# Kernel optimization log

Hardware: AMD Instinct MI355X
Metric: run time of the kernel (lower is better)

## Reference

```python
import jax, jax.numpy as jnp
import numpy as np

N = 4096  # query nodes
L = 4096  # source nodes
C = 512   # in_channels == out_channels (required by the original code path)
H = 8     # num_heads
DK = C // H  # 64


def setup_inputs() -> dict:
    key = jax.random.key(0)
    ks = jax.random.split(key, 12)
    s = 1.0 / np.sqrt(C)
    return {
        "query_input": jax.random.normal(ks[0], (N, C), jnp.float32),
        "source_input": jax.random.normal(ks[1], (L, C), jnp.float32),
        # outer value projection (TransConvLayerGAT.Wv): C -> C
        "Wv_out_w": jax.random.uniform(ks[2], (C, C), jnp.float32, -s, s),
        "Wv_out_b": jax.random.uniform(ks[3], (C,), jnp.float32, -s, s),
        # attention projections
        "Wq_w": jax.random.uniform(ks[4], (C, H * DK), jnp.float32, -s, s),
        "Wq_b": jax.random.uniform(ks[5], (H * DK,), jnp.float32, -s, s),
        "Wk_w": jax.random.uniform(ks[6], (C, H * DK), jnp.float32, -s, s),
        "Wk_b": jax.random.uniform(ks[7], (H * DK,), jnp.float32, -s, s),
        # attention value projection: C -> H * out_channels
        "Wv_attn_w": jax.random.uniform(ks[8], (C, H * C), jnp.float32, -s, s),
        "Wv_attn_b": jax.random.uniform(ks[9], (H * C,), jnp.float32, -s, s),
    }


def reference(query_input, source_input, Wv_out_w, Wv_out_b,
              Wq_w, Wq_b, Wk_w, Wk_b, Wv_attn_w, Wv_attn_b):
    # outer value projection (use_weight=True)
    value = source_input @ Wv_out_w + Wv_out_b            # [L, C]
    # attention projections
    q = (query_input @ Wq_w + Wq_b).reshape(N, H, DK)     # [N, H, DK]
    k = (source_input @ Wk_w + Wk_b).reshape(L, H, DK)    # [L, H, DK]
    v = (value @ Wv_attn_w + Wv_attn_b).reshape(L, H, C)  # [L, H, C]
    scale = 1.0 / jnp.sqrt(jnp.float32(DK))
    scores = jnp.einsum('nhm,lhm->nlh', q, k) * scale     # [N, L, H]
    # NOTE: faithful to original — softmax over the HEADS axis (dim=-1)
    w = jax.nn.softmax(scores, axis=-1)                   # [N, L, H]
    out = jnp.einsum('nlh,lhd->nhd', w, v)                # [N, H, C]
    return out
```

## Files before the change

### kernel.cpp

```cpp
#include <hip/hip_runtime.h>
#include <cstddef>
#include <cstdint>

#define NQ 4096
#define NS 4096
#define CH 512
#define NH 8
#define HC 4096

typedef unsigned short u16;
typedef __attribute__((ext_vector_type(8))) short short8;
typedef __attribute__((ext_vector_type(4))) float f32x4;

__device__ __forceinline__ u16 f2b(float f) {
  unsigned u = __float_as_uint(f);
  return (u16)((u + 0x7fffu + ((u >> 16) & 1u)) >> 16);
}
__device__ __forceinline__ f32x4 mfma16(short8 a, short8 b, f32x4 c) {
  return __builtin_amdgcn_mfma_f32_16x16x32_bf16(a, b, c, 0, 0, 0);
}
__device__ __forceinline__ void gload_lds16(const void* g, void* l) {
  __builtin_amdgcn_global_load_lds(
      (const __attribute__((address_space(1))) void*)g,
      (__attribute__((address_space(3))) void*)l, 16, 0, 0);
}

__global__ __launch_bounds__(256) void convert_flat(
    const float* __restrict__ in, u16* __restrict__ out, int n4)
{
  int idx = blockIdx.x * 256 + threadIdx.x;
  int stride = gridDim.x * 256;
  for (int i = idx; i < n4; i += stride) {
    float4 v = ((const float4*)in)[i];
    ushort4 o;
    o.x = f2b(v.x); o.y = f2b(v.y); o.z = f2b(v.z); o.w = f2b(v.w);
    ((ushort4*)out)[i] = o;
  }
}

__global__ __launch_bounds__(256) void transpose_convert(
    const float* __restrict__ in, u16* __restrict__ out, int R, int C)
{
  __shared__ u16 tile[32][33];
  int tid = threadIdx.x;
  int tx = tid & 31, ty = tid >> 5;
#pragma unroll
  for (int i = 0; i < 4; ++i) {
    int r = blockIdx.y * 32 + ty + i * 8;
    int c = blockIdx.x * 32 + tx;
    tile[ty + i * 8][tx] = f2b(in[(size_t)r * C + c]);
  }
  __syncthreads();
#pragma unroll
  for (int i = 0; i < 4; ++i) {
    int co = blockIdx.x * 32 + ty + i * 8;
    int ro = blockIdx.y * 32 + tx;
    out[(size_t)co * R + ro] = tile[tx][ty + i * 8];
  }
}

__global__ __launch_bounds__(256) void make_bcomb(
    const float* __restrict__ Wva_w, const float* __restrict__ Wvo_b,
    const float* __restrict__ Wva_b, float* __restrict__ bcomb)
{
  int hc = blockIdx.x * 256 + threadIdx.x;
  float s = Wva_b[hc];
  for (int c = 0; c < CH; ++c) s += Wvo_b[c] * Wva_w[(size_t)c * HC + hc];
  bcomb[hc] = s;
}

template <int MODE>
__global__ __launch_bounds__(256) void gemm_core(
    const u16* __restrict__ A, int lda,
    const u16* __restrict__ Bt, int ldb,
    u16* __restrict__ Cb, float* __restrict__ Cf, int ldc,
    const float* __restrict__ bias,
    int K, size_t aPlane, int accum)
{
  constexpr int BM = 128, BN = 128;
  constexpr int FM = 4, FN = 4;
  constexpr int ABYTES = BM * 64;
  constexpr int NCH = (BM + BN) * 64 / 1024;

  __shared__ u16 smem[(BM + BN) * 32];
  u16* As = smem;
  u16* Bs = smem + BM * 32;

  const int tid = threadIdx.x;
  const int wid = tid >> 6, lane = tid & 63;
  const int wr = wid >> 1, wc = wid & 1;
  const int fr = wr * FM * 16, fc = wc * FN * 16;

  int m0, n0;
  if constexpr (MODE == 3) {
    const int bid = blockIdx.x;
    const int z = bid & 7, loc = bid >> 3;
    m0 = (loc >> 2) * BM;
    n0 = (loc & 3) * BN;
    A += (size_t)z * aPlane;
    Bt += (size_t)z * 512 * ldb;
    Cf += (size_t)z * 512;
  } else {
    m0 = blockIdx.y * BM;
    n0 = blockIdx.x * BN;
  }

  f32x4 acc[FM][FN];
#pragma unroll
  for (int m = 0; m < FM; ++m)
#pragma unroll
    for (int n = 0; n < FN; ++n)
#pragma unroll
      for (int i = 0; i < 4; ++i) acc[m][n][i] = 0.f;

  const int lcol = (lane & 3) << 3;
  const int lrow4 = lane >> 2;

  for (int k0 = 0; k0 < K; k0 += 32) {
    for (int c = wid; c < NCH; c += 4) {
      int boff = c << 10;
      const u16* g;
      if (boff < ABYTES) {
        int r = (boff >> 6) + lrow4;
        g = A + (size_t)(m0 + r) * lda + (k0 + lcol);
      } else {
        int r = ((boff - ABYTES) >> 6) + lrow4;
        g = Bt + (size_t)(n0 + r) * ldb + (k0 + lcol);
      }
      gload_lds16(g, (char*)smem + boff);
    }
    __syncthreads();

    short8 af[FM], bq[FN];
    const int kg = (lane >> 4) << 3;
#pragma unroll
    for (int m = 0; m < FM; ++m)
      af[m] = *(const short8*)(As + (size_t)(fr + m * 16 + (lane & 15)) * 32 + kg);
#pragma unroll
    for (int n = 0; n < FN; ++n)
      bq[n] = *(const short8*)(Bs + (size_t)(fc + n * 16 + (lane & 15)) * 32 + kg);
#pragma unroll
    for (int m = 0; m < FM; ++m)
#pragma unroll
      for (int n = 0; n < FN; ++n)
        acc[m][n] = mfma16(af[m], bq[n], acc[m][n]);
    __syncthreads();
  }

  const int crow = (lane >> 4) << 2;
  const int ccol = lane & 15;

  if constexpr (MODE == 0) {
#pragma unroll
    for (int n = 0; n < FN; ++n) {
      int gn = n0 + fc + n * 16 + ccol;
      float bv = bias[gn];
#pragma unroll
      for (int m = 0; m < FM; ++m)
#pragma unroll
        for (int i = 0; i < 4; ++i) {
          int gm = m0 + fr + m * 16 + crow + i;
          Cb[(size_t)gm * ldc + gn] = f2b(acc[m][n][i] + bv);
        }
    }
  } else if constexpr (MODE == 2) {
#pragma unroll
    for (int m = 0; m < FM; ++m)
#pragma unroll
      for (int i = 0; i < 4; ++i) {
        int gm = m0 + fr + m * 16 + crow + i;
        float bv = bias[gm];
#pragma unroll
        for (int n = 0; n < FN; ++n) {
          int gn = n0 + fc + n * 16 + ccol;
          Cb[(size_t)gm * ldc + gn] = f2b(acc[m][n][i] + bv);
        }
      }
  } else if constexpr (MODE == 5) {
#pragma unroll
    for (int m = 0; m < FM; ++m)
#pragma unroll
      for (int i = 0; i < 4; ++i) {
        int gm = m0 + fr + m * 16 + crow + i;
#pragma unroll
        for (int n = 0; n < FN; ++n) {
          int gn = n0 + fc + n * 16 + ccol;
          Cb[(size_t)gm * ldc + gn] = f2b(acc[m][n][i]);
        }
      }
  } else {
#pragma unroll
    for (int m = 0; m < FM; ++m)
#pragma unroll
      for (int i = 0; i < 4; ++i) {
        int gm = m0 + fr + m * 16 + crow + i;
#pragma unroll
        for (int n = 0; n < FN; ++n) {
          int gn = n0 + fc + n * 16 + ccol;
          size_t idx = (size_t)gm * ldc + gn;
          float v = acc[m][n][i];
          if (accum) v += Cf[idx];
          Cf[idx] = v;
        }
      }
  }
}

__global__ __launch_bounds__(256) void attn_pass1(
    const u16* __restrict__ q, const u16* __restrict__ kmat,
    u16* __restrict__ W, int lbase, int LCH, size_t plane)
{
  __shared__ u16 lbuf[16384];
  char* lb = (char*)lbuf;

  const int tid = threadIdx.x, wid = tid >> 6, lane = tid & 63;
  const int n0 = blockIdx.y * 16;
  const int l0 = blockIdx.x * 128;
  const int lw = lbase + l0 + wid * 32;
  const int r16 = lane & 15, g = lane >> 4;
  const int kg = g << 3;

  short8 qf[16];
  const u16* qrow = q + (size_t)(n0 + r16) * CH + kg;
#pragma unroll
  for (int h = 0; h < 8; ++h)
#pragma unroll
    for (int kk = 0; kk < 2; ++kk)
      qf[h * 2 + kk] = *(const short8*)(qrow + h * 64 + kk * 32);

  f32x4 acc[8][2];
#pragma unroll
  for (int h = 0; h < 8; ++h)
#pragma unroll
    for (int f = 0; f < 2; ++f)
#pragma unroll
      for (int i = 0; i < 4; ++i) acc[h][f][i] = 0.f;

#pragma unroll
  for (int f = 0; f < 2; ++f) {
    const u16* krow = kmat + (size_t)(lw + f * 16 + r16) * CH + kg;
#pragma unroll
    for (int h = 0; h < 8; ++h)
#pragma unroll
      for (int kk = 0; kk < 2; ++kk) {
        short8 kf = *(const short8*)(krow + h * 64 + kk * 32);
        acc[h][f] = mfma16(kf, qf[h * 2 + kk], acc[h][f]);
      }
  }

  const int nn = r16;
#pragma unroll
  for (int f = 0; f < 2; ++f) {
    u16 wb[4][8];
#pragma unroll
    for (int i = 0; i < 4; ++i) {
      float s[8], mx = -3e38f;
#pragma unroll
      for (int h = 0; h < 8; ++h) { s[h] = acc[h][f][i] * 0.125f; mx = fmaxf(mx, s[h]); }
      float sum = 0.f;
#pragma unroll
      for (int h = 0; h < 8; ++h) { s[h] = __expf(s[h] - mx); sum += s[h]; }
      float inv = 1.0f / sum;
#pragma unroll
      for (int h = 0; h < 8; ++h) wb[i][h] = f2b(s[h] * inv);
    }
    const int lloc = wid * 32 + f * 16 + g * 4;
#pragma unroll
    for (int h = 0; h < 8; ++h) {
      unsigned p0 = (unsigned)wb[0][h] | ((unsigned)wb[1][h] << 16);
      unsigned p1 = (unsigned)wb[2][h] | ((unsigned)wb[3][h] << 16);
      int wa = (h << 12) + (nn << 8) + (lloc << 1);
      wa ^= (nn & 7) << 4;
      *(uint2*)(lb + wa) = make_uint2(p0, p1);
    }
  }
  __syncthreads();

  const int rn = tid >> 4, rl = (tid & 15) << 3;
#pragma unroll
  for (int h = 0; h < 8; ++h) {
    int ra = (h << 12) + (rn << 8) + (rl << 1);
    ra ^= (rn & 7) << 4;
    uint4 v = *(const uint4*)(lb + ra);
    *(uint4*)(W + (size_t)h * plane + (size_t)(n0 + rn) * LCH + l0 + rl) = v;
  }
}

extern "C" void kernel_launch(void* const* d_in, const int* in_sizes, int n_in,
                              void* d_out, int out_size, void* d_ws, size_t ws_size,
                              hipStream_t stream)
{
  const float* query   = (const float*)d_in[0];
  const float* source  = (const float*)d_in[1];
  const float* Wvo_w   = (const float*)d_in[2];
  const float* Wvo_b   = (const float*)d_in[3];
  const float* Wq_w    = (const float*)d_in[4];
  const float* Wq_b    = (const float*)d_in[5];
  const float* Wk_w    = (const float*)d_in[6];
  const float* Wk_b    = (const float*)d_in[7];
  const float* Wva_w   = (const float*)d_in[8];
  const float* Wva_b   = (const float*)d_in[9];
  float* out = (float*)d_out;

  char* base = (char*)d_ws;
  size_t o = 0;
  auto alloc = [&](size_t b) -> char* {
    char* p = base + o;
    o += (b + 255) & ~(size_t)255;
    return p;
  };
  u16* query_bf  = (u16*)alloc((size_t)NQ * CH * 2);
  u16* source_bf = (u16*)alloc((size_t)NS * CH * 2);
  u16* WqT     = (u16*)alloc((size_t)CH * CH * 2);
  u16* WkT     = (u16*)alloc((size_t)CH * CH * 2);
  u16* WvaT    = (u16*)alloc((size_t)CH * HC * 2);
  u16* Wvo_bf  = (u16*)alloc((size_t)CH * CH * 2);
  u16* WcombT  = (u16*)alloc((size_t)HC * CH * 2);
  float* bcomb = (float*)alloc((size_t)HC * 4);
  u16* qb   = (u16*)alloc((size_t)NQ * CH * 2);
  u16* kb   = (u16*)alloc((size_t)NS * CH * 2);
  u16* V2T  = (u16*)alloc((size_t)HC * NS * 2);
  size_t fixed = o;

  int c = 32;
  for (int cand = 1; cand <= 32; cand <<= 1) {
    if (fixed + (size_t)NH * NQ * (NS / cand) * 2 <= ws_size) { c = cand; break; }
  }
  const int LCH = NS / c;
  u16* Wb = (u16*)alloc((size_t)NH * NQ * LCH * 2);
  const size_t plane = (size_t)NQ * LCH;

  convert_flat<<<1024, 256, 0, stream>>>(query, query_bf, NQ * CH / 4);
  convert_flat<<<1024, 256, 0, stream>>>(source, source_bf, NS * CH / 4);
  convert_flat<<<256, 256, 0, stream>>>(Wvo_w, Wvo_bf, CH * CH / 4);
  transpose_convert<<<dim3(16, 16), 256, 0, stream>>>(Wq_w, WqT, CH, CH);
  transpose_convert<<<dim3(16, 16), 256, 0, stream>>>(Wk_w, WkT, CH, CH);
  transpose_convert<<<dim3(128, 16), 256, 0, stream>>>(Wva_w, WvaT, CH, HC);
  make_bcomb<<<16, 256, 0, stream>>>(Wva_w, Wvo_b, Wva_b, bcomb);

  gemm_core<5><<<dim3(4, 32), 256, 0, stream>>>(WvaT, CH, Wvo_bf, CH, WcombT, nullptr, CH,
                                                nullptr, CH, 0, 0);

  gemm_core<0><<<dim3(4, 32), 256, 0, stream>>>(query_bf, CH, WqT, CH, qb, nullptr, CH,
                                                Wq_b, CH, 0, 0);
  gemm_core<0><<<dim3(4, 32), 256, 0, stream>>>(source_bf, CH, WkT, CH, kb, nullptr, CH,
                                                Wk_b, CH, 0, 0);

  gemm_core<2><<<dim3(32, 32), 256, 0, stream>>>(WcombT, CH, source_bf, CH, V2T, nullptr, NS,
                                                 bcomb, CH, 0, 0);

  for (int ci = 0; ci < c; ++ci) {
    const int lbase = ci * LCH;
    attn_pass1<<<dim3(LCH / 128, NQ / 16), 256, 0, stream>>>(qb, kb, Wb, lbase, LCH, plane);
    gemm_core<3><<<1024, 256, 0, stream>>>(Wb, LCH, V2T + lbase, NS, nullptr, out, HC,
                                           nullptr, LCH, plane, ci > 0 ? 1 : 0);
  }
}
```

Measured before the change: 659.5 us.

## Add double-buffered pass2 GEMM kernel and force at least four L chunks

Splits the batched attention-value GEMM (MODE 3) out into a dedicated kernel that double-buffers LDS tiles with async global-to-LDS loads, so the next K slice loads while MFMAs run on the current one. It also makes the chunk count over source nodes start at 4 instead of 1, which shrinks the intermediate weight buffer and keeps it more cache resident, at the cost of more kernel launches and more read-modify-write passes over the fp32 output.

```diff
diff --git a/kernel.cpp b/kernel.cpp
--- a/kernel.cpp
+++ b/kernel.cpp
@@ -73,9 +73,9 @@
 __global__ __launch_bounds__(256) void gemm_core(
     const u16* __restrict__ A, int lda,
     const u16* __restrict__ Bt, int ldb,
-    u16* __restrict__ Cb, float* __restrict__ Cf, int ldc,
+    u16* __restrict__ Cb, int ldc,
     const float* __restrict__ bias,
-    int K, size_t aPlane, int accum)
+    int K)
 {
   constexpr int BM = 128, BN = 128;
   constexpr int FM = 4, FN = 4;
@@ -90,20 +90,7 @@
   const int wid = tid >> 6, lane = tid & 63;
   const int wr = wid >> 1, wc = wid & 1;
   const int fr = wr * FM * 16, fc = wc * FN * 16;
-
-  int m0, n0;
-  if constexpr (MODE == 3) {
-    const int bid = blockIdx.x;
-    const int z = bid & 7, loc = bid >> 3;
-    m0 = (loc >> 2) * BM;
-    n0 = (loc & 3) * BN;
-    A += (size_t)z * aPlane;
-    Bt += (size_t)z * 512 * ldb;
-    Cf += (size_t)z * 512;
-  } else {
-    m0 = blockIdx.y * BM;
-    n0 = blockIdx.x * BN;
-  }
+  const int m0 = blockIdx.y * BM, n0 = blockIdx.x * BN;
 
   f32x4 acc[FM][FN];
 #pragma unroll
@@ -176,7 +163,7 @@
           Cb[(size_t)gm * ldc + gn] = f2b(acc[m][n][i] + bv);
         }
       }
-  } else if constexpr (MODE == 5) {
+  } else {
 #pragma unroll
     for (int m = 0; m < FM; ++m)
 #pragma unroll
@@ -188,22 +175,110 @@
           Cb[(size_t)gm * ldc + gn] = f2b(acc[m][n][i]);
         }
       }
-  } else {
-#pragma unroll
-    for (int m = 0; m < FM; ++m)
-#pragma unroll
-      for (int i = 0; i < 4; ++i) {
-        int gm = m0 + fr + m * 16 + crow + i;
-#pragma unroll
-        for (int n = 0; n < FN; ++n) {
-          int gn = n0 + fc + n * 16 + ccol;
-          size_t idx = (size_t)gm * ldc + gn;
-          float v = acc[m][n][i];
-          if (accum) v += Cf[idx];
-          Cf[idx] = v;
-        }
-      }
-  }
+  }
+}
+
+__global__ __launch_bounds__(256) void gemm_pass2(
+    const u16* __restrict__ A, int lda,
+    const u16* __restrict__ Bt, int ldb,
+    float* __restrict__ Cf, int ldc,
+    int K, size_t aPlane, int accum)
+{
+  constexpr int BM = 128, BN = 128, BK = 32;
+  constexpr int ABYTES = BM * 64;
+
+  __shared__ u16 smem[2][(BM + BN) * BK];
+
+  const int tid = threadIdx.x;
+  const int wid = tid >> 6, lane = tid & 63;
+  const int wr = wid >> 1, wc = wid & 1;
+  const int fr = wr * 64, fc = wc * 64;
+
+  const int bid = blockIdx.x;
+  const int z = bid & 7, loc = bid >> 3;
+  const int m0 = (loc >> 2) * BM;
+  const int n0 = (loc & 3) * BN;
+  A += (size_t)z * aPlane;
+  Bt += (size_t)z * 512 * ldb;
+  Cf += (size_t)z * 512;
+
+  f32x4 acc[4][4];
+#pragma unroll
+  for (int m = 0; m < 4; ++m)
+#pragma unroll
+    for (int n = 0; n < 4; ++n)
+#pragma unroll
+      for (int i = 0; i < 4; ++i) acc[m][n][i] = 0.f;
+
+  const int lcol = (lane & 3) << 3;
+  const int lrow4 = lane >> 2;
+  const int kg = (lane >> 4) << 3;
+
+  auto stage = [&](int buf, int k0) {
+#pragma unroll
+    for (int c = 0; c < 4; ++c) {
+      int boff = (c * 4 + wid) << 10;
+      const u16* g;
+      if (boff < ABYTES) {
+        int r = (boff >> 6) + lrow4;
+        g = A + (size_t)(m0 + r) * lda + (k0 + lcol);
+      } else {
+        int r = ((boff - ABYTES) >> 6) + lrow4;
+        g = Bt + (size_t)(n0 + r) * ldb + (k0 + lcol);
+      }
+      gload_lds16(g, (char*)smem[buf] + boff);
+    }
+  };
+
+  const int nt = K / BK;
+  stage(0, 0);
+
+  for (int t = 0; t < nt; ++t) {
+    const int cur = t & 1;
+    if (t + 1 < nt) {
+      stage(cur ^ 1, (t + 1) * BK);
+      asm volatile("s_waitcnt vmcnt(4)" ::: "memory");
+    } else {
+      asm volatile("s_waitcnt vmcnt(0)" ::: "memory");
+    }
+    __builtin_amdgcn_s_barrier();
+    __builtin_amdgcn_sched_barrier(0);
+
+    const u16* As = smem[cur];
+    const u16* Bs = smem[cur] + BM * 32;
+    short8 af[4], bq[4];
+#pragma unroll
+    for (int m = 0; m < 4; ++m)
+      af[m] = *(const short8*)(As + (size_t)(fr + m * 16 + (lane & 15)) * 32 + kg);
+#pragma unroll
+    for (int n = 0; n < 4; ++n)
+      bq[n] = *(const short8*)(Bs + (size_t)(fc + n * 16 + (lane & 15)) * 32 + kg);
+#pragma unroll
+    for (int m = 0; m < 4; ++m)
+#pragma unroll
+      for (int n = 0; n < 4; ++n)
+        acc[m][n] = mfma16(af[m], bq[n], acc[m][n]);
+
+    __builtin_amdgcn_sched_barrier(0);
+    __builtin_amdgcn_s_barrier();
+  }
+
+  const int crow = (lane >> 4) << 2;
+  const int ccol = lane & 15;
+#pragma unroll
+  for (int m = 0; m < 4; ++m)
+#pragma unroll
+    for (int i = 0; i < 4; ++i) {
+      int gm = m0 + fr + m * 16 + crow + i;
+#pragma unroll
+      for (int n = 0; n < 4; ++n) {
+        int gn = n0 + fc + n * 16 + ccol;
+        size_t idx = (size_t)gm * ldc + gn;
+        float v = acc[m][n][i];
+        if (accum) v += Cf[idx];
+        Cf[idx] = v;
+      }
+    }
 }
 
 __global__ __launch_bounds__(256) void attn_pass1(
@@ -323,7 +398,7 @@
   size_t fixed = o;
 
   int c = 32;
-  for (int cand = 1; cand <= 32; cand <<= 1) {
+  for (int cand = 4; cand <= 32; cand <<= 1) {
     if (fixed + (size_t)NH * NQ * (NS / cand) * 2 <= ws_size) { c = cand; break; }
   }
   const int LCH = NS / c;
@@ -338,21 +413,21 @@
   transpose_convert<<<dim3(128, 16), 256, 0, stream>>>(Wva_w, WvaT, CH, HC);
   make_bcomb<<<16, 256, 0, stream>>>(Wva_w, Wvo_b, Wva_b, bcomb);
 
-  gemm_core<5><<<dim3(4, 32), 256, 0, stream>>>(WvaT, CH, Wvo_bf, CH, WcombT, nullptr, CH,
-                                                nullptr, CH, 0, 0);
-
-  gemm_core<0><<<dim3(4, 32), 256, 0, stream>>>(query_bf, CH, WqT, CH, qb, nullptr, CH,
-                                                Wq_b, CH, 0, 0);
-  gemm_core<0><<<dim3(4, 32), 256, 0, stream>>>(source_bf, CH, WkT, CH, kb, nullptr, CH,
-                                                Wk_b, CH, 0, 0);
-
-  gemm_core<2><<<dim3(32, 32), 256, 0, stream>>>(WcombT, CH, source_bf, CH, V2T, nullptr, NS,
-                                                 bcomb, CH, 0, 0);
+  gemm_core<5><<<dim3(4, 32), 256, 0, stream>>>(WvaT, CH, Wvo_bf, CH, WcombT, CH,
+                                                nullptr, CH);
+
+  gemm_core<0><<<dim3(4, 32), 256, 0, stream>>>(query_bf, CH, WqT, CH, qb, CH,
+                                                Wq_b, CH);
+  gemm_core<0><<<dim3(4, 32), 256, 0, stream>>>(source_bf, CH, WkT, CH, kb, CH,
+                                                Wk_b, CH);
+
+  gemm_core<2><<<dim3(32, 32), 256, 0, stream>>>(WcombT, CH, source_bf, CH, V2T, NS,
+                                                 bcomb, CH);
 
   for (int ci = 0; ci < c; ++ci) {
     const int lbase = ci * LCH;
     attn_pass1<<<dim3(LCH / 128, NQ / 16), 256, 0, stream>>>(qb, kb, Wb, lbase, LCH, plane);
-    gemm_core<3><<<1024, 256, 0, stream>>>(Wb, LCH, V2T + lbase, NS, nullptr, out, HC,
-                                           nullptr, LCH, plane, ci > 0 ? 1 : 0);
-  }
-}
+    gemm_pass2<<<1024, 256, 0, stream>>>(Wb, LCH, V2T + lbase, NS, out, HC,
+                                         LCH, plane, ci > 0 ? 1 : 0);
+  }
+}
```

Result: no change. 654.3 us (-0.8%).
